# Optimization experiments

Measured on AMD Instinct MI355X. Metric: run time of the kernel, lower is better.

The kernel has to match this reference:

```python
import jax, jax.numpy as jnp
import numpy as np
import math

D_MODEL = 1024
NUM_HEADS = 16
HEAD_DIM = D_MODEL // NUM_HEADS
THETA = 10000.0
B, S = 2, 2048


def _rope(x, positions, theta):
    # x: (b, h, s, d); positions: (s,) int
    d = x.shape[-1]
    inv_freq = theta ** (-jnp.arange(0, d, 2, dtype=jnp.float32) / d)  # (d/2,)
    ang = positions.astype(jnp.float32)[:, None] * inv_freq[None, :]   # (s, d/2)
    cos, sin = jnp.cos(ang), jnp.sin(ang)
    x1 = x[..., ::2]
    x2 = x[..., 1::2]
    r1 = x1 * cos - x2 * sin
    r2 = x1 * sin + x2 * cos
    # interleave back to (..., d)
    return jnp.stack([r1, r2], axis=-1).reshape(x.shape)


def setup_inputs() -> dict:
    key = jax.random.key(0)
    ks = jax.random.split(key, 5)
    std = math.sqrt(2.0 / (D_MODEL + D_MODEL))
    return {
        "x": jax.random.normal(ks[0], (B, S, D_MODEL), dtype=jnp.float32),
        "token_positions": jnp.arange(S, dtype=jnp.int32),
        "Wq": jax.random.normal(ks[1], (D_MODEL, D_MODEL), dtype=jnp.float32) * std,
        "Wk": jax.random.normal(ks[2], (D_MODEL, D_MODEL), dtype=jnp.float32) * std,
        "Wv": jax.random.normal(ks[3], (D_MODEL, D_MODEL), dtype=jnp.float32) * std,
        "Wo": jax.random.normal(ks[4], (D_MODEL, D_MODEL), dtype=jnp.float32) * std,
    }


def reference(x, token_positions, Wq, Wk, Wv, Wo):
    b, s, _ = x.shape
    def split_heads(t):
        return t.reshape(b, s, NUM_HEADS, HEAD_DIM).transpose(0, 2, 1, 3)  # (b,h,s,d)
    Q = split_heads(x @ Wq.T)
    K = split_heads(x @ Wk.T)
    V = split_heads(x @ Wv.T)
    Q = _rope(Q, token_positions, THETA)
    K = _rope(K, token_positions, THETA)
    scores = jnp.einsum("bhqd,bhkd->bhqk", Q, K) / math.sqrt(HEAD_DIM)
    causal = jnp.tril(jnp.ones((s, s), dtype=bool))
    scores = jnp.where(causal, scores, -jnp.inf)
    attn = jax.nn.softmax(scores, axis=-1)
    out = jnp.einsum("bhqk,bhkd->bhqd", attn, V)
    out = out.transpose(0, 2, 1, 3).reshape(b, s, D_MODEL)
    return out @ Wo.T
```

## Files before the change

### kernel.cpp

```cpp
#include <hip/hip_runtime.h>
#include <math.h>

typedef unsigned short u16;
typedef unsigned int   u32;
typedef __attribute__((ext_vector_type(8))) short bf16x8;
typedef __attribute__((ext_vector_type(4))) float floatx4;
typedef __attribute__((ext_vector_type(4))) _Float16 halfx4;
typedef __attribute__((ext_vector_type(8))) _Float16 halfx8;
typedef __attribute__((ext_vector_type(2))) unsigned int uintx2;

#define SEQ 2048
#define DM  1024
#define NH  16
#define DH  64
#define MM  4096
#define QSCALE 0.18033688011112042f

__device__ __forceinline__ u16 f2bf(float f) {
    u32 u = __builtin_bit_cast(u32, f);
    u += 0x7fffu + ((u >> 16) & 1u);
    return (u16)(u >> 16);
}

__device__ __forceinline__ void async16(const void* g, void* l) {
    __builtin_amdgcn_global_load_lds(
        (const __attribute__((address_space(1))) void*)g,
        (__attribute__((address_space(3))) void*)l, 16, 0, 0);
}

__global__ __launch_bounds__(256) void prep_kernel(const float* __restrict__ x,
                                                   const float* __restrict__ w0,
                                                   const float* __restrict__ w1,
                                                   const float* __restrict__ w2,
                                                   const float* __restrict__ w3,
                                                   u16* __restrict__ Xsh,
                                                   u16* __restrict__ Wsh,
                                                   const int* __restrict__ pos,
                                                   float2* __restrict__ tab) {
    const int bid = blockIdx.x, cb = blockIdx.y, tid = threadIdx.x;

    int lin = bid * 16 + cb;
    if (lin < 256) {
        int i = lin * 256 + tid;
        int p = i >> 5, d2 = i & 31;
        float freq = __expf(-(float)d2 * (9.2103403719761836f / 32.0f));
        float sv, cv;
        sincosf((float)pos[p] * freq, &sv, &cv);
        tab[i] = make_float2(cv, sv);
    }

    const float* src; u16* dst; int row0;
    if (bid < 64) { src = x; dst = Xsh; row0 = bid * 64; }
    else {
        int wi = (bid - 64) >> 4;
        src = (wi == 0) ? w0 : (wi == 1) ? w1 : (wi == 2) ? w2 : w3;
        dst = Wsh + (size_t)wi * DM * DM;
        row0 = ((bid - 64) & 15) * 64;
    }
    __shared__ __align__(16) u16 t[64 * 64];
#pragma unroll
    for (int rep = 0; rep < 4; ++rep) {
        int f = rep * 256 + tid;
        int r = f >> 4, c4 = f & 15;
        float4 v = *(const float4*)&src[(size_t)(row0 + r) * DM + cb * 64 + c4 * 4];
        uint2 pk;
        pk.x = (u32)f2bf(v.x) | ((u32)f2bf(v.y) << 16);
        pk.y = (u32)f2bf(v.z) | ((u32)f2bf(v.w) << 16);
        int ch = (c4 >> 1) ^ (r & 7);
        *(uint2*)&t[r * 64 + ch * 8 + (c4 & 1) * 4] = pk;
    }
    __syncthreads();
#pragma unroll
    for (int rep = 0; rep < 2; ++rep) {
        int s = rep * 256 + tid;
        int tile = s >> 6, l = s & 63;
        int mt = tile >> 1, kt = tile & 1, lm = l & 15, quad = l >> 4;
        int m = mt * 16 + lm;
        uint4 v = *(const uint4*)&t[m * 64 + ((kt * 4 + quad) ^ (m & 7)) * 8];
        size_t rowblk = (size_t)(row0 >> 4) + mt;
        size_t ktile  = cb * 2 + kt;
        *(uint4*)&dst[(rowblk * 32 + ktile) * 512 + l * 8] = v;
    }
}

template<int MREP, bool OUTF32>
__global__ __launch_bounds__(256, (MREP == 4) ? 3 : 2)
void gemm_s(const u16* __restrict__ Ash,
            const u16* __restrict__ Wbase,
            u16* __restrict__ qout,
            float* __restrict__ outf,
            _Float16* __restrict__ vtout,
            u16* __restrict__ kout,
            const float2* __restrict__ ropetab) {
    constexpr int BM  = MREP * 32;
    constexpr int AC  = 2 * MREP;
    constexpr int APW = AC / 4;
    constexpr int STEP = (AC + 8) * 512;
    constexpr int SHN  = 3 * STEP;

    const int z  = blockIdx.z;
    const u16* Wp = Wbase + (size_t)z * (DM * DM);
    const int m0 = blockIdx.x * BM, n0 = blockIdx.y * 128;
    const int tid = threadIdx.x, lane = tid & 63, w = tid >> 6;
    const int wr = w >> 1, wc = w & 1;
    const int lm = lane & 15, quad = lane >> 4;
    const int rb0 = m0 >> 4, cb0 = n0 >> 4;

    __shared__ __align__(16) u16 sh[SHN];

    auto stage = [&](int buf, int it) {
        u16* la = sh + buf * STEP;
        u16* lb = la + AC * 512;
#pragma unroll
        for (int j = 0; j < APW; ++j) {
            int c = w * APW + j;
            async16(Ash + ((size_t)(rb0 + c) * 32 + it) * 512 + lane * 8,
                    &la[c * 512 + lane * 8]);
        }
#pragma unroll
        for (int j = 0; j < 2; ++j) {
            int c = w * 2 + j;
            async16(Wp + ((size_t)(cb0 + c) * 32 + it) * 512 + lane * 8,
                    &lb[c * 512 + lane * 8]);
        }
    };

    floatx4 acc[MREP][4];
    const floatx4 z4 = {0.f, 0.f, 0.f, 0.f};
#pragma unroll
    for (int mt = 0; mt < MREP; ++mt)
#pragma unroll
        for (int nt = 0; nt < 4; ++nt) acc[mt][nt] = z4;

    stage(0, 0);
    stage(1, 1);

    int cur = 0;
    for (int it = 0; it < 32; ++it) {
        if (it == 31) {
            asm volatile("s_waitcnt vmcnt(0)\n\ts_barrier" ::: "memory");
        } else {
            if constexpr (MREP == 4)
                asm volatile("s_waitcnt vmcnt(4)\n\ts_barrier" ::: "memory");
            else
                asm volatile("s_waitcnt vmcnt(3)\n\ts_barrier" ::: "memory");
        }
        if (it < 30) {
            int pre = cur - 1; if (pre < 0) pre = 2;
            stage(pre, it + 2);
        }
        const u16* la = sh + cur * STEP;
        const u16* lb = la + AC * 512;
        bf16x8 a[MREP], b[4];
#pragma unroll
        for (int mt = 0; mt < MREP; ++mt)
            a[mt] = *(const bf16x8*)&la[(wr * MREP + mt) * 512 + lane * 8];
#pragma unroll
        for (int nt = 0; nt < 4; ++nt)
            b[nt] = *(const bf16x8*)&lb[(wc * 4 + nt) * 512 + lane * 8];
#pragma unroll
        for (int mt = 0; mt < MREP; ++mt)
#pragma unroll
            for (int nt = 0; nt < 4; ++nt)
                acc[mt][nt] = __builtin_amdgcn_mfma_f32_16x16x32_bf16(
                    a[mt], b[nt], acc[mt][nt], 0, 0, 0);
        ++cur; if (cur == 3) cur = 0;
    }
    __syncthreads();

    if constexpr (OUTF32) {
#pragma unroll
        for (int mt = 0; mt < MREP; ++mt)
#pragma unroll
            for (int r = 0; r < 4; ++r) {
                int row = m0 + wr * (MREP * 16) + mt * 16 + quad * 4 + r;
#pragma unroll
                for (int nt = 0; nt < 4; ++nt) {
                    int col = n0 + wc * 64 + nt * 16 + lm;
                    outf[(size_t)row * DM + col] = acc[mt][nt][r];
                }
            }
        return;
    } else {
        if (z == 0) {
#pragma unroll
            for (int mt = 0; mt < MREP; ++mt)
#pragma unroll
                for (int r = 0; r < 4; ++r) {
                    int row = m0 + wr * (MREP * 16) + mt * 16 + quad * 4 + r;
#pragma unroll
                    for (int nt = 0; nt < 4; ++nt) {
                        int col = n0 + wc * 64 + nt * 16 + lm;
                        float v  = acc[mt][nt][r];
                        float pv = __shfl_xor(v, 1);
                        float2 cs = ropetab[(row & (SEQ - 1)) * 32 + ((col & 63) >> 1)];
                        v = (lm & 1) ? fmaf(pv, cs.y, v * cs.x) : fmaf(v, cs.x, -pv * cs.y);
                        v *= QSCALE;
                        float hv = __shfl_xor(v, 1);
                        if (!(lm & 1)) {
                            u32 pk = (u32)f2bf(v) | ((u32)f2bf(hv) << 16);
                            *(u32*)&qout[(size_t)row * DM + col] = pk;
                        }
                    }
                }
        } else if (z == 1) {
            if constexpr (MREP == 4) {
                u16* t = sh;
#pragma unroll
                for (int mt = 0; mt < MREP; ++mt)
#pragma unroll
                    for (int r = 0; r < 4; ++r) {
                        int rl  = wr * 64 + mt * 16 + quad * 4 + r;
                        int row = m0 + rl;
#pragma unroll
                        for (int nt = 0; nt < 4; ++nt) {
                            int cl  = wc * 64 + nt * 16 + lm;
                            int col = n0 + cl;
                            float v  = acc[mt][nt][r];
                            float pv = __shfl_xor(v, 1);
                            float2 cs = ropetab[(row & (SEQ - 1)) * 32 + ((col & 63) >> 1)];
                            v = (lm & 1) ? fmaf(pv, cs.y, v * cs.x) : fmaf(v, cs.x, -pv * cs.y);
                            t[rl * 136 + cl] = f2bf(v);
                        }
                    }
                __syncthreads();
                {
                    int bb = m0 >> 11;
                    int sblk0 = (m0 & (SEQ - 1)) >> 4;
                    int h0 = n0 >> 6;
#pragma unroll
                    for (int j = 0; j < 8; ++j) {
                        int c = w * 8 + j;
                        int hloc = c >> 4, sblkl = (c >> 1) & 7, ks2 = c & 1;
                        uint4 v4 = *(const uint4*)&t[(sblkl * 16 + lm) * 136 + hloc * 64 + ks2 * 32 + quad * 8];
                        size_t chunk = ((size_t)(bb * NH + h0 + hloc) * 128 + sblk0 + sblkl) * 2 + ks2;
                        *(uint4*)&kout[chunk * 512 + lane * 8] = v4;
                    }
                }
            }
        } else {
            if constexpr (MREP == 4) {
#pragma unroll
                for (int mt = 0; mt < MREP; ++mt) {
                    int row = m0 + wr * 64 + mt * 16;
                    int b = row >> 11;
                    int sblk = (row & (SEQ - 1)) >> 4;
#pragma unroll
                    for (int nt = 0; nt < 4; ++nt) {
                        int col = n0 + wc * 64 + nt * 16;
                        int h = col >> 6;
                        int dblk = (col & 63) >> 4;
                        size_t chunk = ((size_t)(b * NH + h) * 128 + sblk) * 4 + dblk;
                        uint2 pk;
                        pk.x = __builtin_bit_cast(u32, __builtin_amdgcn_cvt_pkrtz(acc[mt][nt][0], acc[mt][nt][1]));
                        pk.y = __builtin_bit_cast(u32, __builtin_amdgcn_cvt_pkrtz(acc[mt][nt][2], acc[mt][nt][3]));
                        *(uint2*)&vtout[chunk * 256 + lane * 4] = pk;
                    }
                }
            }
        }
    }
}

static __device__ const u16 itab[21] = {
    0x0B0A,
    0x0A09,
    0x0908,
    0x280F, 0x708F, 0x6F7E, 0x0807,
    0x270E, 0x270D, 0x6E7D, 0x6D6C, 0x0706,
    0x260C, 0x260B, 0x6C6B, 0x0605,
    0x0504, 0x0403, 0x0302, 0x0201, 0x0100
};

__global__ __launch_bounds__(256, 2) void attn_kernel(const u16* __restrict__ Q,
                                                      const u16* __restrict__ Kf,
                                                      const _Float16* __restrict__ Vf,
                                                      u16* __restrict__ AO,
                                                      _Float16* __restrict__ Opart,
                                                      float* __restrict__ Lpart) {
    const int u  = blockIdx.x;
    const int e  = itab[u >> 5];
    const int bh = u & 31;
    const int qt = e & 15;
    const int k0 = (e >> 4) & 15;
    const int k1 = (e >> 8) & 31;
    const bool split = (e >> 13) & 1;
    const int part = e >> 14;
    const int b  = bh >> 4, h = bh & 15;
    const int q0 = qt * 128;
    const int tid = threadIdx.x, w = tid >> 6, lane = tid & 63;
    const int lm = lane & 15, quad = lane >> 4;

    __shared__ __align__(16) u16      lsK[2][16 * 512];
    __shared__ __align__(16) _Float16 lsV[2][32 * 256];

    bf16x8 qb[2][2];
#pragma unroll
    for (int qi = 0; qi < 2; ++qi)
#pragma unroll
        for (int ks = 0; ks < 2; ++ks)
            qb[qi][ks] = *(const bf16x8*)
                &Q[(size_t)(b * SEQ + q0 + w * 32 + qi * 16 + lm) * DM + h * DH + ks * 32 + quad * 8];

    const floatx4 z4 = {0.f, 0.f, 0.f, 0.f};
    floatx4 o[2][4];
    floatx4 o5[2];
#pragma unroll
    for (int qi = 0; qi < 2; ++qi) {
#pragma unroll
        for (int dt = 0; dt < 4; ++dt) o[qi][dt] = z4;
        o5[qi] = z4;
    }

    const u16*      Kb = Kf + (size_t)bh * (256 * 512);
    const _Float16* Vb = Vf + (size_t)bh * (128 * 4 * 256);

    auto stageKV = [&](int buf, int kt) {
#pragma unroll
        for (int j = 0; j < 4; ++j) {
            int kc = w * 4 + j;
            async16(Kb + ((size_t)kt * 16 + kc) * 512 + lane * 8,
                    &lsK[buf][kc * 512 + lane * 8]);
            int off = w * 2048 + j * 512 + lane * 8;
            async16(Vb + (size_t)kt * 8192 + off, &lsV[buf][off]);
        }
    };

    stageKV(k0 & 1, k0);
    const halfx4 ones = {(_Float16)1.f, (_Float16)1.f, (_Float16)1.f, (_Float16)1.f};

    for (int kt = k0; kt < k1; ++kt) {
        __syncthreads();
        if (kt + 1 < k1) stageKV((kt + 1) & 1, kt + 1);
        const u16*      Lk = lsK[kt & 1];
        const _Float16* Lv = lsV[kt & 1];

        floatx4 s4[2][8];
#pragma unroll
        for (int qi = 0; qi < 2; ++qi)
#pragma unroll
            for (int st = 0; st < 8; ++st) s4[qi][st] = z4;
#pragma unroll
        for (int ks = 0; ks < 2; ++ks)
#pragma unroll
            for (int st = 0; st < 8; ++st) {
                bf16x8 ka = *(const bf16x8*)&Lk[(st * 2 + ks) * 512 + lane * 8];
#pragma unroll
                for (int qi = 0; qi < 2; ++qi)
                    s4[qi][st] = __builtin_amdgcn_mfma_f32_16x16x32_bf16(ka, qb[qi][ks], s4[qi][st], 0, 0, 0);
            }

        const bool diag = (kt == qt);
#pragma unroll
        for (int st = 0; st < 8; ++st) {
            halfx4 pb2[2];
#pragma unroll
            for (int qi = 0; qi < 2; ++qi) {
#pragma unroll
                for (int r = 0; r < 4; ++r) {
                    float v = s4[qi][st][r];
                    if (diag) {
                        int keyloc = st * 16 + quad * 4 + r;
                        if (keyloc > w * 32 + qi * 16 + lm) v = -1e30f;
                    }
                    s4[qi][st][r] = __builtin_amdgcn_exp2f(v);
                }
                uintx2 pk2;
                pk2.x = __builtin_bit_cast(u32, __builtin_amdgcn_cvt_pkrtz(s4[qi][st][0], s4[qi][st][1]));
                pk2.y = __builtin_bit_cast(u32, __builtin_amdgcn_cvt_pkrtz(s4[qi][st][2], s4[qi][st][3]));
                pb2[qi] = __builtin_bit_cast(halfx4, pk2);
            }
#pragma unroll
            for (int dt = 0; dt < 4; ++dt) {
                halfx4 va = *(const halfx4*)&Lv[(st * 4 + dt) * 256 + lane * 4];
#pragma unroll
                for (int qi = 0; qi < 2; ++qi)
                    o[qi][dt] = __builtin_amdgcn_mfma_f32_16x16x16f16(va, pb2[qi], o[qi][dt], 0, 0, 0);
            }
#pragma unroll
            for (int qi = 0; qi < 2; ++qi)
                o5[qi] = __builtin_amdgcn_mfma_f32_16x16x16f16(ones, pb2[qi], o5[qi], 0, 0, 0);
        }
    }

    if (split) {
        const int pi = (bh * 5 + (qt - 11)) * 2 + part;
        _Float16* Od = Opart + (size_t)pi * (128 * 64);
#pragma unroll
        for (int qi = 0; qi < 2; ++qi) {
            const int q = w * 32 + qi * 16 + lm;
#pragma unroll
            for (int dt = 0; dt < 4; ++dt) {
                uintx2 pk2;
                pk2.x = __builtin_bit_cast(u32, __builtin_amdgcn_cvt_pkrtz(o[qi][dt][0], o[qi][dt][1]));
                pk2.y = __builtin_bit_cast(u32, __builtin_amdgcn_cvt_pkrtz(o[qi][dt][2], o[qi][dt][3]));
                *(uintx2*)&Od[(size_t)q * 64 + dt * 16 + quad * 4] = pk2;
            }
            if (quad == 0) Lpart[pi * 128 + q] = o5[qi][0];
        }
        return;
    }

    float rl[2] = {1.0f / o5[0][0], 1.0f / o5[1][0]};

    __syncthreads();
    u16* eb = (u16*)&lsK[0][0];
#pragma unroll
    for (int qi = 0; qi < 2; ++qi) {
        const int q = w * 32 + qi * 16 + lm;
#pragma unroll
        for (int dt = 0; dt < 4; ++dt) {
            uint2 pk;
            pk.x = (u32)f2bf(o[qi][dt][0] * rl[qi]) | ((u32)f2bf(o[qi][dt][1] * rl[qi]) << 16);
            pk.y = (u32)f2bf(o[qi][dt][2] * rl[qi]) | ((u32)f2bf(o[qi][dt][3] * rl[qi]) << 16);
            int ch = (dt * 2 + (quad >> 1)) ^ (lm & 7);
            *(uint2*)&eb[q * 64 + ch * 8 + (quad & 1) * 4] = pk;
        }
    }
    __syncthreads();
    const size_t rowblk0 = (size_t)((b * SEQ + q0) >> 4);
#pragma unroll
    for (int rbi = 0; rbi < 2; ++rbi) {
#pragma unroll
        for (int kt = 0; kt < 2; ++kt) {
            uint4 v = *(const uint4*)&eb[((w * 2 + rbi) * 16 + lm) * 64 + ((kt * 4 + quad) ^ (lm & 7)) * 8];
            *(uint4*)&AO[((rowblk0 + w * 2 + rbi) * 32 + (h * 2 + kt)) * 512 + lane * 8] = v;
        }
    }
}

__global__ __launch_bounds__(256) void combine_kernel(const _Float16* __restrict__ Op,
                                                      const float* __restrict__ Lp,
                                                      u16* __restrict__ AO) {
    const int g = blockIdx.x;
    const int bh = g / 5, qto = g - bh * 5;
    const int qt = 11 + qto;
    const int b = bh >> 4, h = bh & 15;
    const int q0 = qt * 128;
    const int pi0 = g * 2;
    const _Float16* O0 = Op + (size_t)pi0 * (128 * 64);
    const _Float16* O1 = O0 + 128 * 64;
    const float* L0 = Lp + pi0 * 128;
    const float* L1 = L0 + 128;
    const int tid = threadIdx.x;
#pragma unroll
    for (int rep = 0; rep < 4; ++rep) {
        int idx = rep * 256 + tid;
        int chunk = idx >> 6, lane = idx & 63;
        int rb = chunk >> 1, kt2 = chunk & 1;
        int lm = lane & 15, quad = lane >> 4;
        int q = rb * 16 + lm;
        int d = kt2 * 32 + quad * 8;
        float rl = 1.0f / (L0[q] + L1[q]);
        halfx8 a = *(const halfx8*)&O0[(size_t)q * 64 + d];
        halfx8 c = *(const halfx8*)&O1[(size_t)q * 64 + d];
        uint4 v;
        u32 pk[4];
#pragma unroll
        for (int j = 0; j < 4; ++j) {
            float v0 = ((float)a[2 * j]     + (float)c[2 * j])     * rl;
            float v1 = ((float)a[2 * j + 1] + (float)c[2 * j + 1]) * rl;
            pk[j] = (u32)f2bf(v0) | ((u32)f2bf(v1) << 16);
        }
        v.x = pk[0]; v.y = pk[1]; v.z = pk[2]; v.w = pk[3];
        size_t rowblk = ((size_t)(b * SEQ + q0) >> 4) + rb;
        *(uint4*)&AO[(rowblk * 32 + (h * 2 + kt2)) * 512 + lane * 8] = v;
    }
}

extern "C" void kernel_launch(void* const* d_in, const int* in_sizes, int n_in,
                              void* d_out, int out_size, void* d_ws, size_t ws_size,
                              hipStream_t stream) {
    const float* x   = (const float*)d_in[0];
    const int*   pos = (const int*)d_in[1];
    float* out = (float*)d_out;

    u16* ws = (u16*)d_ws;
    const size_t MD = (size_t)MM * DM;
    const size_t DD = (size_t)DM * DM;
    u16* Xsh = ws;
    u16* Wsh = ws + MD;
    u16* Qbf = ws + MD + 4 * DD;
    u16* Kfb = Qbf + MD;
    u16* VtB = Kfb + MD;
    float2* ropetab = (float2*)(VtB + MD);
    _Float16* Vt = (_Float16*)VtB;
    u16* AOsh = Xsh;
    _Float16* Opart = (_Float16*)Wsh;
    float* Lpart = (float*)(ropetab + SEQ * 32);

    prep_kernel<<<dim3(128, 16), 256, 0, stream>>>(
        x, (const float*)d_in[2], (const float*)d_in[3], (const float*)d_in[4],
        (const float*)d_in[5], Xsh, Wsh, pos, ropetab);

    gemm_s<4, false><<<dim3(32, 8, 3), 256, 0, stream>>>(
        Xsh, Wsh, Qbf, nullptr, Vt, Kfb, ropetab);

    attn_kernel<<<dim3(672), 256, 0, stream>>>(Qbf, Kfb, Vt, AOsh, Opart, Lpart);

    combine_kernel<<<dim3(160), 256, 0, stream>>>(Opart, Lpart, AOsh);

    gemm_s<2, true><<<dim3(64, 8, 1), 256, 0, stream>>>(
        AOsh, Wsh + 3 * DD, nullptr, out, nullptr, nullptr, ropetab);
}
```

Before: 174.0 us.

## Use 16x16x32 f16 MFMA for PV and permute K layout to match

The P·V product and row-sum now use the 16x16x32 f16 MFMA, which consumes two 16-key subtiles at once, instead of two 16x16x16 instructions. This halves the PV MFMA instruction count. The K store layout is permuted by key row so the S accumulator lanes line up with the wider PV operand. V fragments are gathered from two halfx4 LDS loads. s_setprio hints are added around the MFMA blocks to favour matrix issue across waves. The change carries correctness risk from the key-row permutation, which must stay consistent between the producer, the causal mask and the V layout.

Result: slower. 180.6 us (+3.8%).

```diff
diff --git a/kernel.cpp b/kernel.cpp
--- a/kernel.cpp
+++ b/kernel.cpp
@@ -232,7 +232,8 @@
                     for (int j = 0; j < 8; ++j) {
                         int c = w * 8 + j;
                         int hloc = c >> 4, sblkl = (c >> 1) & 7, ks2 = c & 1;
-                        uint4 v4 = *(const uint4*)&t[(sblkl * 16 + lm) * 136 + hloc * 64 + ks2 * 32 + quad * 8];
+                        int keyrow = (sblkl >> 1) * 32 + ((lm >> 2) * 8) + ((sblkl & 1) * 4) + (lm & 3);
+                        uint4 v4 = *(const uint4*)&t[keyrow * 136 + hloc * 64 + ks2 * 32 + quad * 8];
                         size_t chunk = ((size_t)(bb * NH + h0 + hloc) * 128 + sblk0 + sblkl) * 2 + ks2;
                         *(uint4*)&kout[chunk * 512 + lane * 8] = v4;
                     }
@@ -327,7 +328,8 @@
     };
 
     stageKV(k0 & 1, k0);
-    const halfx4 ones = {(_Float16)1.f, (_Float16)1.f, (_Float16)1.f, (_Float16)1.f};
+    const halfx8 ones8 = {(_Float16)1.f, (_Float16)1.f, (_Float16)1.f, (_Float16)1.f,
+                          (_Float16)1.f, (_Float16)1.f, (_Float16)1.f, (_Float16)1.f};
 
     for (int kt = k0; kt < k1; ++kt) {
         __syncthreads();
@@ -340,6 +342,7 @@
         for (int qi = 0; qi < 2; ++qi)
 #pragma unroll
             for (int st = 0; st < 8; ++st) s4[qi][st] = z4;
+        __builtin_amdgcn_s_setprio(1);
 #pragma unroll
         for (int ks = 0; ks < 2; ++ks)
 #pragma unroll
@@ -349,37 +352,49 @@
                 for (int qi = 0; qi < 2; ++qi)
                     s4[qi][st] = __builtin_amdgcn_mfma_f32_16x16x32_bf16(ka, qb[qi][ks], s4[qi][st], 0, 0, 0);
             }
+        __builtin_amdgcn_s_setprio(0);
 
         const bool diag = (kt == qt);
 #pragma unroll
-        for (int st = 0; st < 8; ++st) {
-            halfx4 pb2[2];
+        for (int g = 0; g < 4; ++g) {
+            halfx8 pb8[2];
 #pragma unroll
             for (int qi = 0; qi < 2; ++qi) {
 #pragma unroll
-                for (int r = 0; r < 4; ++r) {
-                    float v = s4[qi][st][r];
-                    if (diag) {
-                        int keyloc = st * 16 + quad * 4 + r;
-                        if (keyloc > w * 32 + qi * 16 + lm) v = -1e30f;
+                for (int t = 0; t < 2; ++t) {
+                    int st = g * 2 + t;
+#pragma unroll
+                    for (int r = 0; r < 4; ++r) {
+                        float v = s4[qi][st][r];
+                        if (diag) {
+                            int keyloc = g * 32 + quad * 8 + t * 4 + r;
+                            if (keyloc > w * 32 + qi * 16 + lm) v = -1e30f;
+                        }
+                        s4[qi][st][r] = __builtin_amdgcn_exp2f(v);
                     }
-                    s4[qi][st][r] = __builtin_amdgcn_exp2f(v);
                 }
-                uintx2 pk2;
-                pk2.x = __builtin_bit_cast(u32, __builtin_amdgcn_cvt_pkrtz(s4[qi][st][0], s4[qi][st][1]));
-                pk2.y = __builtin_bit_cast(u32, __builtin_amdgcn_cvt_pkrtz(s4[qi][st][2], s4[qi][st][3]));
-                pb2[qi] = __builtin_bit_cast(halfx4, pk2);
-            }
+                uint4 pk4;
+                pk4.x = __builtin_bit_cast(u32, __builtin_amdgcn_cvt_pkrtz(s4[qi][g * 2][0],     s4[qi][g * 2][1]));
+                pk4.y = __builtin_bit_cast(u32, __builtin_amdgcn_cvt_pkrtz(s4[qi][g * 2][2],     s4[qi][g * 2][3]));
+                pk4.z = __builtin_bit_cast(u32, __builtin_amdgcn_cvt_pkrtz(s4[qi][g * 2 + 1][0], s4[qi][g * 2 + 1][1]));
+                pk4.w = __builtin_bit_cast(u32, __builtin_amdgcn_cvt_pkrtz(s4[qi][g * 2 + 1][2], s4[qi][g * 2 + 1][3]));
+                pb8[qi] = __builtin_bit_cast(halfx8, pk4);
+            }
+            __builtin_amdgcn_s_setprio(1);
 #pragma unroll
             for (int dt = 0; dt < 4; ++dt) {
-                halfx4 va = *(const halfx4*)&Lv[(st * 4 + dt) * 256 + lane * 4];
+                const _Float16* cb = &Lv[(((2 * g + (quad >> 1)) * 4 + dt) * 256) + (quad & 1) * 128 + lm * 4];
+                halfx4 lo = *(const halfx4*)cb;
+                halfx4 hi = *(const halfx4*)(cb + 64);
+                halfx8 va8 = __builtin_shufflevector(lo, hi, 0, 1, 2, 3, 4, 5, 6, 7);
 #pragma unroll
                 for (int qi = 0; qi < 2; ++qi)
-                    o[qi][dt] = __builtin_amdgcn_mfma_f32_16x16x16f16(va, pb2[qi], o[qi][dt], 0, 0, 0);
+                    o[qi][dt] = __builtin_amdgcn_mfma_f32_16x16x32_f16(va8, pb8[qi], o[qi][dt], 0, 0, 0);
             }
 #pragma unroll
             for (int qi = 0; qi < 2; ++qi)
-                o5[qi] = __builtin_amdgcn_mfma_f32_16x16x16f16(ones, pb2[qi], o5[qi], 0, 0, 0);
+                o5[qi] = __builtin_amdgcn_mfma_f32_16x16x32_f16(ones8, pb8[qi], o5[qi], 0, 0, 0);
+            __builtin_amdgcn_s_setprio(0);
         }
     }
 
```
